# Kernel optimization log

Hardware: AMD Instinct MI355X
Metric: run time of the kernel (lower is better)

The kernel has to match this reference:

```python
import jax, jax.numpy as jnp
import numpy as np

ALIGNED_H = 7
ALIGNED_W = 7
IMG_H, IMG_W = 800.0, 1216.0


def setup_inputs() -> dict:
    key = jax.random.key(0)
    k1, k2, k3, k4 = jax.random.split(key, 4)
    N, C, H, W = 2, 256, 200, 304
    R = 2000
    features = jax.random.normal(k1, (N, C, H, W), dtype=jnp.float32)
    # rois: [batch_idx, x1, y1, x2, y2] in image coordinates
    bidx = jax.random.randint(k2, (R,), 0, N).astype(jnp.float32)
    xy1 = jax.random.uniform(k3, (R, 2)) * jnp.array([IMG_W * 0.7, IMG_H * 0.7])
    wh = 16.0 + jax.random.uniform(k4, (R, 2)) * jnp.array([IMG_W * 0.3 - 16.0, IMG_H * 0.3 - 16.0])
    xy2 = jnp.minimum(xy1 + wh, jnp.array([IMG_W - 1.0, IMG_H - 1.0]))
    rois = jnp.concatenate([bidx[:, None], xy1[:, 0:1], xy1[:, 1:2], xy2[:, 0:1], xy2[:, 1:2]], axis=1).astype(jnp.float32)
    spatial_scale = jnp.float32(0.25)
    return {"features": features, "rois": rois, "spatial_scale": spatial_scale}


def roi_align(features, rois, spatial_scale, ah, aw):
    N, C, H, W = features.shape
    b = rois[:, 0].astype(jnp.int32)                       # [R]
    x1 = rois[:, 1] * spatial_scale
    y1 = rois[:, 2] * spatial_scale
    x2 = rois[:, 3] * spatial_scale
    y2 = rois[:, 4] * spatial_scale
    roi_w = jnp.maximum(x2 - x1 + 1.0, 0.0)
    roi_h = jnp.maximum(y2 - y1 + 1.0, 0.0)
    bin_h = roi_h / (ah - 1.0)                             # [R]
    bin_w = roi_w / (aw - 1.0)
    ph = jnp.arange(ah, dtype=jnp.float32)
    pw = jnp.arange(aw, dtype=jnp.float32)
    h = y1[:, None] + ph[None, :] * bin_h[:, None]         # [R, ah]
    w = x1[:, None] + pw[None, :] * bin_w[:, None]         # [R, aw]
    valid = ((h >= 0) & (h < H))[:, :, None] & ((w >= 0) & (w < W))[:, None, :]  # [R, ah, aw]
    hs = jnp.clip(jnp.floor(h), 0.0, H - 2.0)              # kernel: min(floor(h), H-2)
    ws = jnp.clip(jnp.floor(w), 0.0, W - 2.0)
    dh = (h - hs)[:, :, None]                              # [R, ah, 1]
    dw = (w - ws)[:, None, :]                              # [R, 1, aw]
    yi = hs.astype(jnp.int32)[:, :, None]                  # [R, ah, 1]
    xi = ws.astype(jnp.int32)[:, None, :]                  # [R, 1, aw]
    bi = b[:, None, None]                                  # [R, 1, 1]
    # gather 4 corners -> [R, ah, aw, C]
    v00 = features[bi, :, yi, xi]
    v01 = features[bi, :, yi, xi + 1]
    v10 = features[bi, :, yi + 1, xi]
    v11 = features[bi, :, yi + 1, xi + 1]
    dh4 = dh[..., None]
    dw4 = dw[..., None]
    val = (v00 * (1 - dh4) * (1 - dw4) + v01 * (1 - dh4) * dw4
           + v10 * dh4 * (1 - dw4) + v11 * dh4 * dw4)
    out = jnp.where(valid[..., None], val, 0.0)            # [R, ah, aw, C]
    return jnp.transpose(out, (0, 3, 1, 2))                # [R, C, ah, aw]


def reference(features, rois, spatial_scale):
    return roi_align(features, rois, spatial_scale, ALIGNED_H, ALIGNED_W)
```

## Files before the change

### kernel.cpp

```cpp
#include <hip/hip_runtime.h>

#define C_ 256
#define H_ 200
#define W_ 304
#define AH 7
#define AW 7
#define KK 49
#define ROWU 131

typedef float f32x4 __attribute__((ext_vector_type(4)));

__device__ __forceinline__ float h2f(unsigned short s) {
    _Float16 h; __builtin_memcpy(&h, &s, 2); return (float)h;
}
__device__ __forceinline__ unsigned short f2h(float f) {
    _Float16 h = (_Float16)f; unsigned short s; __builtin_memcpy(&s, &h, 2); return s;
}

__global__ __launch_bounds__(256) void transpose_nchw_nhwc_f16(
    const float* __restrict__ in, unsigned short* __restrict__ out) {
    __shared__ unsigned int tile[128][34];
    const int HW = H_ * W_;
    const int n  = blockIdx.z;
    const int p0 = blockIdx.x * 64;
    const int c0 = blockIdx.y * 128;
    const float* inb = in + (size_t)n * C_ * HW;
    unsigned short* outb = out + (size_t)n * HW * C_;

    {
        const int q  = threadIdx.x & 15;
        const int r0 = threadIdx.x >> 4;
        #pragma unroll
        for (int i = 0; i < 8; ++i) {
            const int c = r0 + 16 * i;
            const f32x4 v = __builtin_nontemporal_load(
                (const f32x4*)&inb[(size_t)(c0 + c) * HW + p0 + 4 * q]);
            const unsigned int ulo = (unsigned)f2h(v.x) | ((unsigned)f2h(v.y) << 16);
            const unsigned int uhi = (unsigned)f2h(v.z) | ((unsigned)f2h(v.w) << 16);
            *(uint2*)&tile[c][2 * q] = make_uint2(ulo, uhi);
        }
    }
    __syncthreads();
    {
        const int pp0 = threadIdx.x & 15;
        const int cq  = threadIdx.x >> 4;
        #pragma unroll
        for (int i = 0; i < 2; ++i) {
            const int pp = pp0 + 16 * i;
            unsigned int u[8];
            #pragma unroll
            for (int jj = 0; jj < 8; ++jj) u[jj] = tile[8 * cq + jj][pp];
            unsigned int pe[4], po[4];
            #pragma unroll
            for (int k = 0; k < 4; ++k) {
                pe[k] = (u[2 * k] & 0xFFFFu) | (u[2 * k + 1] << 16);
                po[k] = (u[2 * k] >> 16) | (u[2 * k + 1] & 0xFFFF0000u);
            }
            unsigned short* oA = &outb[(size_t)(p0 + 2 * pp) * C_ + c0 + 8 * cq];
            unsigned short* oB = oA + C_;
            *(uint4*)oA = make_uint4(pe[0], pe[1], pe[2], pe[3]);
            *(uint4*)oB = make_uint4(po[0], po[1], po[2], po[3]);
        }
    }
}

__device__ __forceinline__ void samp(
    const unsigned short* __restrict__ fb, int k,
    float y1, float x1, float bin_h, float bin_w, int c4, float* o) {
    const int ph = k / AW;
    const int pw = k - ph * AW;
    const float h  = y1 + (float)ph * bin_h;
    const float w  = x1 + (float)pw * bin_w;
    const float hs = fminf(fmaxf(floorf(h), 0.0f), (float)(H_ - 2));
    const float ws = fminf(fmaxf(floorf(w), 0.0f), (float)(W_ - 2));
    const float dh = h - hs;
    const float dw = w - ws;
    const int   yi = (int)hs;
    const int   xi = (int)ws;
    const bool  valid = (h >= 0.0f) && (h < (float)H_) &&
                        (w >= 0.0f) && (w < (float)W_);
    const unsigned short* p = fb + ((size_t)yi * W_ + xi) * C_ + c4;
    const ushort4 a00 = *(const ushort4*)p;
    const ushort4 a01 = *(const ushort4*)(p + C_);
    const ushort4 a10 = *(const ushort4*)(p + (size_t)W_ * C_);
    const ushort4 a11 = *(const ushort4*)(p + (size_t)W_ * C_ + C_);
    const float w00 = (1.0f - dh) * (1.0f - dw);
    const float w01 = (1.0f - dh) * dw;
    const float w10 = dh * (1.0f - dw);
    const float w11 = dh * dw;
    o[0] = h2f(a00.x) * w00 + h2f(a01.x) * w01 + h2f(a10.x) * w10 + h2f(a11.x) * w11;
    o[1] = h2f(a00.y) * w00 + h2f(a01.y) * w01 + h2f(a10.y) * w10 + h2f(a11.y) * w11;
    o[2] = h2f(a00.z) * w00 + h2f(a01.z) * w01 + h2f(a10.z) * w10 + h2f(a11.z) * w11;
    o[3] = h2f(a00.w) * w00 + h2f(a01.w) * w01 + h2f(a10.w) * w10 + h2f(a11.w) * w11;
    if (!valid) { o[0] = 0.0f; o[1] = 0.0f; o[2] = 0.0f; o[3] = 0.0f; }
}

__global__ __launch_bounds__(512) void roialign_nhwc_f16(
    const unsigned short* __restrict__ tf, const float* __restrict__ rois,
    const float* __restrict__ scale_ptr, float* __restrict__ out) {
    __shared__ unsigned int shu[KK * ROWU];
    const int r    = blockIdx.x;
    const int wave = threadIdx.x >> 6;
    const int lane = threadIdx.x & 63;
    const int c4   = lane * 4;

    const float scale = scale_ptr[0];
    const float* roi = rois + (size_t)r * 5;
    const int   b  = (int)roi[0];
    const float x1 = roi[1] * scale;
    const float y1 = roi[2] * scale;
    const float x2 = roi[3] * scale;
    const float y2 = roi[4] * scale;
    const float roi_w = fmaxf(x2 - x1 + 1.0f, 0.0f);
    const float roi_h = fmaxf(y2 - y1 + 1.0f, 0.0f);
    const float bin_h = roi_h / (float)(AH - 1);
    const float bin_w = roi_w / (float)(AW - 1);
    const unsigned short* fb = tf + (size_t)b * (H_ * W_) * C_;

    #pragma unroll 2
    for (int k = wave; k < KK; k += 8) {
        float v[4];
        samp(fb, k, y1, x1, bin_h, bin_w, c4, v);
        const unsigned int u0 = (unsigned)f2h(v[0]) | ((unsigned)f2h(v[1]) << 16);
        const unsigned int u1 = (unsigned)f2h(v[2]) | ((unsigned)f2h(v[3]) << 16);
        shu[k * ROWU + 2 * lane]     = u0;
        shu[k * ROWU + 2 * lane + 1] = u1;
    }
    __syncthreads();

    float* ob = out + (size_t)r * (C_ * KK);
    #pragma unroll
    for (int i = 0; i < 25; ++i) {
        const int f = threadIdx.x + 512 * i;
        if (i < 24 || f < C_ * KK) {
            const int c = f / KK;
            const int k = f - c * KK;
            const unsigned int u = shu[k * ROWU + (c >> 1)];
            const unsigned short hv = (c & 1) ? (unsigned short)(u >> 16)
                                              : (unsigned short)(u & 0xFFFFu);
            __builtin_nontemporal_store(h2f(hv), &ob[f]);
        }
    }
}

__global__ __launch_bounds__(256) void roialign_nchw(
    const float* __restrict__ feat, const float* __restrict__ rois,
    const float* __restrict__ scale_ptr, float* __restrict__ out) {
    __shared__ float sout[C_ * KK];
    const int r = blockIdx.x;
    const int c = threadIdx.x;
    const float scale = scale_ptr[0];
    const float* roi = rois + (size_t)r * 5;
    const int   b  = (int)roi[0];
    const float x1 = roi[1] * scale;
    const float y1 = roi[2] * scale;
    const float x2 = roi[3] * scale;
    const float y2 = roi[4] * scale;
    const float roi_w = fmaxf(x2 - x1 + 1.0f, 0.0f);
    const float roi_h = fmaxf(y2 - y1 + 1.0f, 0.0f);
    const float bin_h = roi_h / (float)(AH - 1);
    const float bin_w = roi_w / (float)(AW - 1);
    const float* fb = feat + ((size_t)b * C_ + c) * (H_ * W_);

    for (int ph = 0; ph < AH; ++ph) {
        const float h  = y1 + (float)ph * bin_h;
        const float hs = fminf(fmaxf(floorf(h), 0.0f), (float)(H_ - 2));
        const float dh = h - hs;
        const int   yi = (int)hs;
        const bool  vh = (h >= 0.0f) && (h < (float)H_);
        #pragma unroll
        for (int pw = 0; pw < AW; ++pw) {
            const float w  = x1 + (float)pw * bin_w;
            const float ws = fminf(fmaxf(floorf(w), 0.0f), (float)(W_ - 2));
            const float dw = w - ws;
            const int   xi = (int)ws;
            const bool  valid = vh && (w >= 0.0f) && (w < (float)W_);
            const float v00 = fb[(size_t)yi * W_ + xi];
            const float v01 = fb[(size_t)yi * W_ + xi + 1];
            const float v10 = fb[(size_t)(yi + 1) * W_ + xi];
            const float v11 = fb[(size_t)(yi + 1) * W_ + xi + 1];
            float val = v00 * (1.0f - dh) * (1.0f - dw)
                      + v01 * (1.0f - dh) * dw
                      + v10 * dh * (1.0f - dw)
                      + v11 * dh * dw;
            sout[c * KK + ph * AW + pw] = valid ? val : 0.0f;
        }
    }
    __syncthreads();
    float* ob = out + (size_t)r * C_ * KK;
    #pragma unroll 4
    for (int i = threadIdx.x; i < C_ * KK; i += 256) ob[i] = sout[i];
}

extern "C" void kernel_launch(void* const* d_in, const int* in_sizes, int n_in,
                              void* d_out, int out_size, void* d_ws, size_t ws_size,
                              hipStream_t stream) {
    const float* feat  = (const float*)d_in[0];
    const float* rois  = (const float*)d_in[1];
    const float* scale = (const float*)d_in[2];
    float* out = (float*)d_out;

    const int R = in_sizes[1] / 5;
    const int N = in_sizes[0] / (C_ * H_ * W_);
    const size_t need = (size_t)N * C_ * H_ * W_ * sizeof(unsigned short);

    if (ws_size >= need) {
        unsigned short* tf = (unsigned short*)d_ws;
        dim3 tb(256);
        dim3 tg((H_ * W_) / 64, C_ / 128, N);
        hipLaunchKernelGGL(transpose_nchw_nhwc_f16, tg, tb, 0, stream, feat, tf);
        hipLaunchKernelGGL(roialign_nhwc_f16, dim3(R), dim3(512), 0, stream,
                           tf, rois, scale, out);
    } else {
        hipLaunchKernelGGL(roialign_nchw, dim3(R), dim3(256), 0, stream,
                           feat, rois, scale, out);
    }
}
```

Before: 78.96 us.

## Fuse transpose and ROIAlign into one persistent cooperative kernel with grid sync

```diff
diff --git a/kernel.cpp b/kernel.cpp
--- a/kernel.cpp
+++ b/kernel.cpp
@@ -1,4 +1,6 @@
 #include <hip/hip_runtime.h>
+#include <hip/hip_cooperative_groups.h>
+namespace cg = cooperative_groups;
 
 #define C_ 256
 #define H_ 200
@@ -7,6 +9,7 @@
 #define AW 7
 #define KK 49
 #define ROWU 131
+#define BUFW 6419
 
 typedef float f32x4 __attribute__((ext_vector_type(4)));
 
@@ -15,53 +18,6 @@
 }
 __device__ __forceinline__ unsigned short f2h(float f) {
     _Float16 h = (_Float16)f; unsigned short s; __builtin_memcpy(&s, &h, 2); return s;
-}
-
-__global__ __launch_bounds__(256) void transpose_nchw_nhwc_f16(
-    const float* __restrict__ in, unsigned short* __restrict__ out) {
-    __shared__ unsigned int tile[128][34];
-    const int HW = H_ * W_;
-    const int n  = blockIdx.z;
-    const int p0 = blockIdx.x * 64;
-    const int c0 = blockIdx.y * 128;
-    const float* inb = in + (size_t)n * C_ * HW;
-    unsigned short* outb = out + (size_t)n * HW * C_;
-
-    {
-        const int q  = threadIdx.x & 15;
-        const int r0 = threadIdx.x >> 4;
-        #pragma unroll
-        for (int i = 0; i < 8; ++i) {
-            const int c = r0 + 16 * i;
-            const f32x4 v = __builtin_nontemporal_load(
-                (const f32x4*)&inb[(size_t)(c0 + c) * HW + p0 + 4 * q]);
-            const unsigned int ulo = (unsigned)f2h(v.x) | ((unsigned)f2h(v.y) << 16);
-            const unsigned int uhi = (unsigned)f2h(v.z) | ((unsigned)f2h(v.w) << 16);
-            *(uint2*)&tile[c][2 * q] = make_uint2(ulo, uhi);
-        }
-    }
-    __syncthreads();
-    {
-        const int pp0 = threadIdx.x & 15;
-        const int cq  = threadIdx.x >> 4;
-        #pragma unroll
-        for (int i = 0; i < 2; ++i) {
-            const int pp = pp0 + 16 * i;
-            unsigned int u[8];
-            #pragma unroll
-            for (int jj = 0; jj < 8; ++jj) u[jj] = tile[8 * cq + jj][pp];
-            unsigned int pe[4], po[4];
-            #pragma unroll
-            for (int k = 0; k < 4; ++k) {
-                pe[k] = (u[2 * k] & 0xFFFFu) | (u[2 * k + 1] << 16);
-                po[k] = (u[2 * k] >> 16) | (u[2 * k + 1] & 0xFFFF0000u);
-            }
-            unsigned short* oA = &outb[(size_t)(p0 + 2 * pp) * C_ + c0 + 8 * cq];
-            unsigned short* oB = oA + C_;
-            *(uint4*)oA = make_uint4(pe[0], pe[1], pe[2], pe[3]);
-            *(uint4*)oB = make_uint4(po[0], po[1], po[2], po[3]);
-        }
-    }
 }
 
 __device__ __forceinline__ void samp(
@@ -95,6 +51,151 @@
     if (!valid) { o[0] = 0.0f; o[1] = 0.0f; o[2] = 0.0f; o[3] = 0.0f; }
 }
 
+__global__ __launch_bounds__(512) void roialign_fused(
+    const float* __restrict__ feat, unsigned short* __restrict__ tf,
+    const float* __restrict__ rois, const float* __restrict__ scale_ptr,
+    float* __restrict__ out, int nblocks, int R, int ntile) {
+    __shared__ unsigned int buf[BUFW];
+    const int bid = blockIdx.x;
+    const int HW = H_ * W_;
+
+    for (int tile = bid; tile < ntile; tile += nblocks) {
+        const int px   = tile % 950;
+        const int rest = tile / 950;
+        const int p0 = px * 64;
+        const int c0 = (rest & 1) * 128;
+        const int n  = rest >> 1;
+        const float* inb = feat + (size_t)n * C_ * HW;
+        unsigned short* outb = tf + (size_t)n * HW * C_;
+        __syncthreads();
+        {
+            const int q  = threadIdx.x & 15;
+            const int r0 = threadIdx.x >> 4;
+            #pragma unroll
+            for (int i = 0; i < 4; ++i) {
+                const int c = r0 + 32 * i;
+                const f32x4 v = __builtin_nontemporal_load(
+                    (const f32x4*)&inb[(size_t)(c0 + c) * HW + p0 + 4 * q]);
+                const unsigned int ulo = (unsigned)f2h(v.x) | ((unsigned)f2h(v.y) << 16);
+                const unsigned int uhi = (unsigned)f2h(v.z) | ((unsigned)f2h(v.w) << 16);
+                *(uint2*)&buf[c * 34 + 2 * q] = make_uint2(ulo, uhi);
+            }
+        }
+        __syncthreads();
+        {
+            const int pp = threadIdx.x & 31;
+            const int cq = threadIdx.x >> 5;
+            unsigned int u[8];
+            #pragma unroll
+            for (int jj = 0; jj < 8; ++jj) u[jj] = buf[(8 * cq + jj) * 34 + pp];
+            unsigned int pe[4], po[4];
+            #pragma unroll
+            for (int k = 0; k < 4; ++k) {
+                pe[k] = (u[2 * k] & 0xFFFFu) | (u[2 * k + 1] << 16);
+                po[k] = (u[2 * k] >> 16) | (u[2 * k + 1] & 0xFFFF0000u);
+            }
+            unsigned short* oA = &outb[(size_t)(p0 + 2 * pp) * C_ + c0 + 8 * cq];
+            unsigned short* oB = oA + C_;
+            *(uint4*)oA = make_uint4(pe[0], pe[1], pe[2], pe[3]);
+            *(uint4*)oB = make_uint4(po[0], po[1], po[2], po[3]);
+        }
+    }
+
+    __threadfence();
+    cg::this_grid().sync();
+
+    const float scale = scale_ptr[0];
+    const int wave = threadIdx.x >> 6;
+    const int lane = threadIdx.x & 63;
+    const int c4   = lane * 4;
+
+    for (int r = bid; r < R; r += nblocks) {
+        const float* roi = rois + (size_t)r * 5;
+        const int   b  = (int)roi[0];
+        const float x1 = roi[1] * scale;
+        const float y1 = roi[2] * scale;
+        const float x2 = roi[3] * scale;
+        const float y2 = roi[4] * scale;
+        const float roi_w = fmaxf(x2 - x1 + 1.0f, 0.0f);
+        const float roi_h = fmaxf(y2 - y1 + 1.0f, 0.0f);
+        const float bin_h = roi_h / (float)(AH - 1);
+        const float bin_w = roi_w / (float)(AW - 1);
+        const unsigned short* fb = tf + (size_t)b * (H_ * W_) * C_;
+
+        __syncthreads();
+        #pragma unroll 2
+        for (int k = wave; k < KK; k += 8) {
+            float v[4];
+            samp(fb, k, y1, x1, bin_h, bin_w, c4, v);
+            const unsigned int u0 = (unsigned)f2h(v[0]) | ((unsigned)f2h(v[1]) << 16);
+            const unsigned int u1 = (unsigned)f2h(v[2]) | ((unsigned)f2h(v[3]) << 16);
+            buf[k * ROWU + 2 * lane]     = u0;
+            buf[k * ROWU + 2 * lane + 1] = u1;
+        }
+        __syncthreads();
+
+        float* ob = out + (size_t)r * (C_ * KK);
+        #pragma unroll
+        for (int i = 0; i < 25; ++i) {
+            const int f = threadIdx.x + 512 * i;
+            if (i < 24 || f < C_ * KK) {
+                const int c = f / KK;
+                const int k = f - c * KK;
+                const unsigned int u = buf[k * ROWU + (c >> 1)];
+                const unsigned short hv = (c & 1) ? (unsigned short)(u >> 16)
+                                                  : (unsigned short)(u & 0xFFFFu);
+                __builtin_nontemporal_store(h2f(hv), &ob[f]);
+            }
+        }
+    }
+}
+
+__global__ __launch_bounds__(256) void transpose_nchw_nhwc_f16(
+    const float* __restrict__ in, unsigned short* __restrict__ out) {
+    __shared__ unsigned int tile[128][34];
+    const int HW = H_ * W_;
+    const int n  = blockIdx.z;
+    const int p0 = blockIdx.x * 64;
+    const int c0 = blockIdx.y * 128;
+    const float* inb = in + (size_t)n * C_ * HW;
+    unsigned short* outb = out + (size_t)n * HW * C_;
+    {
+        const int q  = threadIdx.x & 15;
+        const int r0 = threadIdx.x >> 4;
+        #pragma unroll
+        for (int i = 0; i < 8; ++i) {
+            const int c = r0 + 16 * i;
+            const f32x4 v = __builtin_nontemporal_load(
+                (const f32x4*)&inb[(size_t)(c0 + c) * HW + p0 + 4 * q]);
+            const unsigned int ulo = (unsigned)f2h(v.x) | ((unsigned)f2h(v.y) << 16);
+            const unsigned int uhi = (unsigned)f2h(v.z) | ((unsigned)f2h(v.w) << 16);
+            *(uint2*)&tile[c][2 * q] = make_uint2(ulo, uhi);
+        }
+    }
+    __syncthreads();
+    {
+        const int pp0 = threadIdx.x & 15;
+        const int cq  = threadIdx.x >> 4;
+        #pragma unroll
+        for (int i = 0; i < 2; ++i) {
+            const int pp = pp0 + 16 * i;
+            unsigned int u[8];
+            #pragma unroll
+            for (int jj = 0; jj < 8; ++jj) u[jj] = tile[8 * cq + jj][pp];
+            unsigned int pe[4], po[4];
+            #pragma unroll
+            for (int k = 0; k < 4; ++k) {
+                pe[k] = (u[2 * k] & 0xFFFFu) | (u[2 * k + 1] << 16);
+                po[k] = (u[2 * k] >> 16) | (u[2 * k + 1] & 0xFFFF0000u);
+            }
+            unsigned short* oA = &outb[(size_t)(p0 + 2 * pp) * C_ + c0 + 8 * cq];
+            unsigned short* oB = oA + C_;
+            *(uint4*)oA = make_uint4(pe[0], pe[1], pe[2], pe[3]);
+            *(uint4*)oB = make_uint4(po[0], po[1], po[2], po[3]);
+        }
+    }
+}
+
 __global__ __launch_bounds__(512) void roialign_nhwc_f16(
     const unsigned short* __restrict__ tf, const float* __restrict__ rois,
     const float* __restrict__ scale_ptr, float* __restrict__ out) {
@@ -103,7 +204,6 @@
     const int wave = threadIdx.x >> 6;
     const int lane = threadIdx.x & 63;
     const int c4   = lane * 4;
-
     const float scale = scale_ptr[0];
     const float* roi = rois + (size_t)r * 5;
     const int   b  = (int)roi[0];
@@ -127,7 +227,6 @@
         shu[k * ROWU + 2 * lane + 1] = u1;
     }
     __syncthreads();
-
     float* ob = out + (size_t)r * (C_ * KK);
     #pragma unroll
     for (int i = 0; i < 25; ++i) {
@@ -161,7 +260,6 @@
     const float bin_h = roi_h / (float)(AH - 1);
     const float bin_w = roi_w / (float)(AW - 1);
     const float* fb = feat + ((size_t)b * C_ + c) * (H_ * W_);
-
     for (int ph = 0; ph < AH; ++ph) {
         const float h  = y1 + (float)ph * bin_h;
         const float hs = fminf(fmaxf(floorf(h), 0.0f), (float)(H_ - 2));
@@ -206,6 +304,20 @@
 
     if (ws_size >= need) {
         unsigned short* tf = (unsigned short*)d_ws;
+        int maxb = 0;
+        hipError_t qe = hipOccupancyMaxActiveBlocksPerMultiprocessor(
+            &maxb, (const void*)roialign_fused, 512, 0);
+        int G = (qe == hipSuccess) ? maxb * 256 : 0;
+        if (G > 1024) G = 1024;
+        if (G >= 256) {
+            int ntile = 950 * 2 * N;
+            void* args[] = { (void*)&feat, (void*)&tf, (void*)&rois,
+                             (void*)&scale, (void*)&out,
+                             (void*)&G, (void*)&R, (void*)&ntile };
+            hipError_t le = hipLaunchCooperativeKernel(
+                (const void*)roialign_fused, dim3(G), dim3(512), args, 0, stream);
+            if (le == hipSuccess) return;
+        }
         dim3 tb(256);
         dim3 tg((H_ * W_) / 64, C_ / 128, N);
         hipLaunchKernelGGL(transpose_nchw_nhwc_f16, tg, tb, 0, stream, feat, tf);
```

Measured after the change: 196.9 us. +149.3%, slower.

## Gather adjacent pixel pairs with 16-byte loads and cross-lane shuffle in RoIAlign

Applied to the files above, without the earlier changes.

```diff
diff --git a/kernel.cpp b/kernel.cpp
--- a/kernel.cpp
+++ b/kernel.cpp
@@ -64,37 +64,6 @@
     }
 }
 
-__device__ __forceinline__ void samp(
-    const unsigned short* __restrict__ fb, int k,
-    float y1, float x1, float bin_h, float bin_w, int c4, float* o) {
-    const int ph = k / AW;
-    const int pw = k - ph * AW;
-    const float h  = y1 + (float)ph * bin_h;
-    const float w  = x1 + (float)pw * bin_w;
-    const float hs = fminf(fmaxf(floorf(h), 0.0f), (float)(H_ - 2));
-    const float ws = fminf(fmaxf(floorf(w), 0.0f), (float)(W_ - 2));
-    const float dh = h - hs;
-    const float dw = w - ws;
-    const int   yi = (int)hs;
-    const int   xi = (int)ws;
-    const bool  valid = (h >= 0.0f) && (h < (float)H_) &&
-                        (w >= 0.0f) && (w < (float)W_);
-    const unsigned short* p = fb + ((size_t)yi * W_ + xi) * C_ + c4;
-    const ushort4 a00 = *(const ushort4*)p;
-    const ushort4 a01 = *(const ushort4*)(p + C_);
-    const ushort4 a10 = *(const ushort4*)(p + (size_t)W_ * C_);
-    const ushort4 a11 = *(const ushort4*)(p + (size_t)W_ * C_ + C_);
-    const float w00 = (1.0f - dh) * (1.0f - dw);
-    const float w01 = (1.0f - dh) * dw;
-    const float w10 = dh * (1.0f - dw);
-    const float w11 = dh * dw;
-    o[0] = h2f(a00.x) * w00 + h2f(a01.x) * w01 + h2f(a10.x) * w10 + h2f(a11.x) * w11;
-    o[1] = h2f(a00.y) * w00 + h2f(a01.y) * w01 + h2f(a10.y) * w10 + h2f(a11.y) * w11;
-    o[2] = h2f(a00.z) * w00 + h2f(a01.z) * w01 + h2f(a10.z) * w10 + h2f(a11.z) * w11;
-    o[3] = h2f(a00.w) * w00 + h2f(a01.w) * w01 + h2f(a10.w) * w10 + h2f(a11.w) * w11;
-    if (!valid) { o[0] = 0.0f; o[1] = 0.0f; o[2] = 0.0f; o[3] = 0.0f; }
-}
-
 __global__ __launch_bounds__(512) void roialign_nhwc_f16(
     const unsigned short* __restrict__ tf, const float* __restrict__ rois,
     const float* __restrict__ scale_ptr, float* __restrict__ out) {
@@ -102,7 +71,6 @@
     const int r    = blockIdx.x;
     const int wave = threadIdx.x >> 6;
     const int lane = threadIdx.x & 63;
-    const int c4   = lane * 4;
 
     const float scale = scale_ptr[0];
     const float* roi = rois + (size_t)r * 5;
@@ -117,14 +85,56 @@
     const float bin_w = roi_w / (float)(AW - 1);
     const unsigned short* fb = tf + (size_t)b * (H_ * W_) * C_;
 
-    #pragma unroll 2
-    for (int k = wave; k < KK; k += 8) {
-        float v[4];
-        samp(fb, k, y1, x1, bin_h, bin_w, c4, v);
-        const unsigned int u0 = (unsigned)f2h(v[0]) | ((unsigned)f2h(v[1]) << 16);
-        const unsigned int u1 = (unsigned)f2h(v[2]) | ((unsigned)f2h(v[3]) << 16);
-        shu[k * ROWU + 2 * lane]     = u0;
-        shu[k * ROWU + 2 * lane + 1] = u1;
+    const int base = (49 * wave) >> 3;
+    #pragma unroll
+    for (int j = 0; j < 7; ++j) {
+        const int k  = base + j;
+        const int ph = k / AW;
+        const int pw = k - ph * AW;
+        const float h  = y1 + (float)ph * bin_h;
+        const float w  = x1 + (float)pw * bin_w;
+        const float hs = fminf(fmaxf(floorf(h), 0.0f), (float)(H_ - 2));
+        const float ws = fminf(fmaxf(floorf(w), 0.0f), (float)(W_ - 2));
+        const float dh = h - hs;
+        const float dw = w - ws;
+        const int   yi = (int)hs;
+        const int   xi = (int)ws;
+        const bool  valid = (h >= 0.0f) && (h < (float)H_) &&
+                            (w >= 0.0f) && (w < (float)W_);
+        const uint4* rowA = (const uint4*)(fb + (((size_t)yi * W_ + xi) << 8));
+        const uint4* rowB = rowA + ((size_t)W_ << 5);
+        const uint4 a = rowA[lane];
+        const uint4 bq = rowB[lane];
+        unsigned int yp[4];
+        float ylo[4], yhi[4];
+        #pragma unroll
+        for (int d = 0; d < 4; ++d) {
+            const unsigned int ua = (&a.x)[d];
+            const unsigned int ub = (&bq.x)[d];
+            const float alo = h2f((unsigned short)(ua & 0xFFFFu));
+            const float ahi = h2f((unsigned short)(ua >> 16));
+            const float blo = h2f((unsigned short)(ub & 0xFFFFu));
+            const float bhi = h2f((unsigned short)(ub >> 16));
+            ylo[d] = alo + dh * (blo - alo);
+            yhi[d] = ahi + dh * (bhi - ahi);
+            yp[d] = (unsigned)f2h(ylo[d]) | ((unsigned)f2h(yhi[d]) << 16);
+        }
+        unsigned int xq[4];
+        #pragma unroll
+        for (int d = 0; d < 4; ++d) xq[d] = (unsigned)__shfl_xor((int)yp[d], 32, 64);
+        if (lane < 32) {
+            unsigned int wq[4];
+            #pragma unroll
+            for (int d = 0; d < 4; ++d) {
+                const float plo = h2f((unsigned short)(xq[d] & 0xFFFFu));
+                const float phi = h2f((unsigned short)(xq[d] >> 16));
+                float olo = ylo[d] + dw * (plo - ylo[d]);
+                float ohi = yhi[d] + dw * (phi - yhi[d]);
+                if (!valid) { olo = 0.0f; ohi = 0.0f; }
+                wq[d] = (unsigned)f2h(olo) | ((unsigned)f2h(ohi) << 16);
+            }
+            *(uint4*)&shu[k * ROWU + 4 * lane] = make_uint4(wq[0], wq[1], wq[2], wq[3]);
+        }
     }
     __syncthreads();
 
@@ -161,7 +171,6 @@
     const float bin_h = roi_h / (float)(AH - 1);
     const float bin_w = roi_w / (float)(AW - 1);
     const float* fb = feat + ((size_t)b * C_ + c) * (H_ * W_);
-
     for (int ph = 0; ph < AH; ++ph) {
         const float h  = y1 + (float)ph * bin_h;
         const float hs = fminf(fmaxf(floorf(h), 0.0f), (float)(H_ - 2));
```

Result: slower. 84.11 us (+6.5%).
